# Kernel optimization log

Measured on AMD Instinct MI355X. Metric: run time of the kernel, lower is better.

The kernel has to match this reference:

```python
import jax, jax.numpy as jnp
import numpy as np

N = 100000
IN_DIM = 1280
HID = 128
EPS = 1e-5

def _gconv(x, src, dst, W, b, n):
    # DGL GraphConv, norm='both': D_out^{-1/2} gather -> sum -> D_in^{-1/2}, then W, b.
    # Project first (in_feats >= out_feats here) so edge messages are HID-dim.
    ones = jnp.ones(src.shape[0], dtype=x.dtype)
    out_deg = jnp.clip(jax.ops.segment_sum(ones, src, num_segments=n), 1.0)
    in_deg = jnp.clip(jax.ops.segment_sum(ones, dst, num_segments=n), 1.0)
    h = (x * (out_deg ** -0.5)[:, None]) @ W          # [n, HID]
    agg = jax.ops.segment_sum(h[src], dst, num_segments=n)  # scatter-add over edges
    return agg * (in_deg ** -0.5)[:, None] + b

def _batchnorm(x, g, b):
    m = x.mean(0)
    v = jnp.mean((x - m) ** 2, axis=0)  # biased variance (torch BN normalization)
    return (x - m) * jax.lax.rsqrt(v + EPS) * g + b

def _layer(x, edges, W, b, fcW, fcb, g, beta, n):
    # HeteroGraphConv aggregate='sum' over 3 relations, then FC + ReLU + BN
    h = _gconv(x, edges[0][0], edges[0][1], W[0], b[0], n)
    h = h + _gconv(x, edges[1][0], edges[1][1], W[1], b[1], n)
    h = h + _gconv(x, edges[2][0], edges[2][1], W[2], b[2], n)
    h = h @ fcW + fcb
    h = jax.nn.relu(h)
    return _batchnorm(h, g, beta)

def setup_inputs() -> dict:
    key = jax.random.key(0)
    ks = jax.random.split(key, 16)
    x = jax.random.normal(ks[0], (N, IN_DIM), dtype=jnp.float32)
    seq_edges = jax.random.randint(ks[1], (2, 200000), 0, N, dtype=jnp.int32)
    knn_edges = jax.random.randint(ks[2], (2, 1000000), 0, N, dtype=jnp.int32)
    dis_edges = jax.random.randint(ks[3], (2, 1600000), 0, N, dtype=jnp.int32)
    s_in = 1.0 / np.sqrt(IN_DIM)
    s_h = 1.0 / np.sqrt(HID)
    W0 = jax.random.normal(ks[4], (3, IN_DIM, HID), dtype=jnp.float32) * s_in
    b0 = jnp.zeros((3, HID), dtype=jnp.float32)
    fcW0 = jax.random.normal(ks[5], (HID, HID), dtype=jnp.float32) * s_h
    fcb0 = jnp.zeros((HID,), dtype=jnp.float32)
    g0 = jnp.ones((HID,), dtype=jnp.float32)
    beta0 = jnp.zeros((HID,), dtype=jnp.float32)
    W1 = jax.random.normal(ks[6], (3, HID, HID), dtype=jnp.float32) * s_h
    b1 = jnp.zeros((3, HID), dtype=jnp.float32)
    fcW1 = jax.random.normal(ks[7], (HID, HID), dtype=jnp.float32) * s_h
    fcb1 = jnp.zeros((HID,), dtype=jnp.float32)
    g1 = jnp.ones((HID,), dtype=jnp.float32)
    beta1 = jnp.zeros((HID,), dtype=jnp.float32)
    return {"x": x, "seq_edges": seq_edges, "knn_edges": knn_edges, "dis_edges": dis_edges,
            "W0": W0, "b0": b0, "fcW0": fcW0, "fcb0": fcb0, "g0": g0, "beta0": beta0,
            "W1": W1, "b1": b1, "fcW1": fcW1, "fcb1": fcb1, "g1": g1, "beta1": beta1}

def reference(x, seq_edges, knn_edges, dis_edges,
              W0, b0, fcW0, fcb0, g0, beta0,
              W1, b1, fcW1, fcb1, g1, beta1):
    edges = [seq_edges, knn_edges, dis_edges]
    n = x.shape[0]
    h = _layer(x, edges, W0, b0, fcW0, fcb0, g0, beta0, n)
    # dropout after non-final layers is identity at eval
    h = _layer(h, edges, W1, b1, fcW1, fcb1, g1, beta1, n)
    return h
```

## Files before the change

kernel.cpp:

```cpp
#include <hip/hip_runtime.h>
#include <hip/hip_bf16.h>
#include <math.h>

#define NN 100000
#define HID 128
#define EPSV 1e-5f

typedef short bf16x8 __attribute__((ext_vector_type(8)));
typedef float f32x4 __attribute__((ext_vector_type(4)));
typedef unsigned short u16;

__device__ __forceinline__ u16 f2b(float f) {
  unsigned u = __builtin_bit_cast(unsigned, f);
  u += 0x7FFFu + ((u >> 16) & 1u);
  return (u16)(u >> 16);
}
__device__ __forceinline__ float b2f(u16 h) {
  unsigned u = ((unsigned)h) << 16;
  return __builtin_bit_cast(float, u);
}

#define AS1(p) ((__attribute__((address_space(1))) void*)(p))
#define AS3(p) ((__attribute__((address_space(3))) void*)(p))

static __global__ void k_init(float* __restrict__ degs, int n6,
                              int* __restrict__ cur, int nc,
                              float* __restrict__ stats, int ns) {
  int i = blockIdx.x * blockDim.x + threadIdx.x;
  if (i < n6) degs[i] = 0.f;
  if (i < nc) cur[i] = 0;
  if (i < ns) stats[i] = 0.f;
}

static __global__ void k_deg_all(const int* __restrict__ seq, const int* __restrict__ knn,
                                 const int* __restrict__ dis, int E0, int E1, int E2,
                                 float* __restrict__ sOut, float* __restrict__ sIn) {
  int e = blockIdx.x * blockDim.x + threadIdx.x;
  int rel, eo;
  const int *src, *dst;
  if (e < E0)            { rel = 0; eo = e;           src = seq; dst = seq + E0; }
  else if (e < E0 + E1)  { rel = 1; eo = e - E0;      src = knn; dst = knn + E1; }
  else if (e < E0+E1+E2) { rel = 2; eo = e - E0 - E1; src = dis; dst = dis + E2; }
  else return;
  atomicAdd(&sOut[(size_t)rel * NN + src[eo]], 1.f);
  atomicAdd(&sIn[(size_t)rel * NN + dst[eo]], 1.f);
}

static __global__ void k_scan1_c(const float* __restrict__ indegRaw, int* __restrict__ out,
                                 int* __restrict__ aux, int n) {
  __shared__ int s[256];
  int t = threadIdx.x, i = blockIdx.x * 256 + t;
  int v = 0;
  if (i < NN) v = (int)(indegRaw[i] + indegRaw[NN + i] + indegRaw[2 * NN + i]);
  s[t] = v; __syncthreads();
#pragma unroll
  for (int d = 1; d < 256; d <<= 1) {
    int x = (t >= d) ? s[t - d] : 0;
    __syncthreads();
    s[t] += x;
    __syncthreads();
  }
  if (i < n) out[i] = s[t] - v;
  if (t == 255) aux[blockIdx.x] = s[255];
}

static __global__ void k_scan2(int* __restrict__ aux, int nb) {
  __shared__ int s[256];
  __shared__ int carry;
  int t = threadIdx.x;
  if (t == 0) carry = 0;
  __syncthreads();
  for (int base = 0; base < nb; base += 256) {
    int i = base + t;
    int v = (i < nb) ? aux[i] : 0;
    s[t] = v; __syncthreads();
#pragma unroll
    for (int d = 1; d < 256; d <<= 1) {
      int x = (t >= d) ? s[t - d] : 0;
      __syncthreads();
      s[t] += x;
      __syncthreads();
    }
    int excl = s[t] - v + carry;
    if (i < nb) aux[i] = excl;
    int tot = s[255];
    __syncthreads();
    if (t == 0) carry += tot;
    __syncthreads();
  }
}

static __global__ void k_scan3(int* __restrict__ out, const int* __restrict__ aux, int n) {
  int i = blockIdx.x * 256 + threadIdx.x;
  if (i < n) out[i] += aux[blockIdx.x];
}

static __global__ void k_fill_all(const int* __restrict__ seq, const int* __restrict__ knn,
                                  const int* __restrict__ dis, int E0, int E1, int E2,
                                  const int* __restrict__ off, int* __restrict__ cur,
                                  int* __restrict__ srt) {
  int e = blockIdx.x * blockDim.x + threadIdx.x;
  int rel, eo;
  const int *src, *dst;
  if (e < E0)            { rel = 0; eo = e;           src = seq; dst = seq + E0; }
  else if (e < E0 + E1)  { rel = 1; eo = e - E0;      src = knn; dst = knn + E1; }
  else if (e < E0+E1+E2) { rel = 2; eo = e - E0 - E1; src = dis; dst = dis + E2; }
  else return;
  int d = dst[eo];
  int p = off[d] + atomicAdd(&cur[d], 1);
  srt[p] = (src[eo] << 2) | rel;
}

static __global__ void k_cvt_all(const float* __restrict__ W0, const float* __restrict__ W1,
                                 const float* __restrict__ fcW0, const float* __restrict__ fcW1,
                                 u16* __restrict__ Wt0, u16* __restrict__ Wt1,
                                 u16* __restrict__ fcWt0, u16* __restrict__ fcWt1) {
  const int N0 = 3 * 1280 * 128, N1 = 3 * 128 * 128, N2 = 128 * 128;
  int i = blockIdx.x * blockDim.x + threadIdx.x;
  if (i < N0) {
    int rel = i / (1280 * 128);
    int rem = i - rel * 1280 * 128;
    int k = rem >> 7, c = rem & 127;
    Wt0[((size_t)rel * 128 + c) * 1280 + k] = f2b(W0[i]);
  } else if (i < N0 + N1) {
    int j = i - N0;
    int rel = j / (128 * 128);
    int rem = j - rel * 128 * 128;
    int k = rem >> 7, c = rem & 127;
    Wt1[((size_t)rel * 128 + c) * 128 + k] = f2b(W1[j]);
  } else if (i < N0 + N1 + N2) {
    int j = i - N0 - N1;
    int k = j >> 7, c = j & 127;
    fcWt0[c * 128 + k] = f2b(fcW0[j]);
  } else if (i < N0 + N1 + 2 * N2) {
    int j = i - N0 - N1 - N2;
    int k = j >> 7, c = j & 127;
    fcWt1[c * 128 + k] = f2b(fcW1[j]);
  }
}

template<int K, bool AF32, bool AFFINE>
__global__ __launch_bounds__(512)
void k_gemm_pipe(const void* __restrict__ Av,
                 const u16* __restrict__ Wt,
                 const float* __restrict__ soutRaw,
                 const float* __restrict__ abg,
                 u16* __restrict__ Y,
                 int M)
{
  constexpr int A_BYTES = AF32 ? (128 * 32 * 4) : (128 * 32 * 2);
  constexpr int B_BYTES = 384 * 32 * 2;
  constexpr int BUF_U16 = (A_BYTES + B_BYTES) / 2;
  __shared__ u16 lds[3][BUF_U16];
  __shared__ float abl[256];

  const int row0 = blockIdx.x * 128;
  const int t    = threadIdx.x;
  const int lane = t & 63;
  const int w    = t >> 6;
  const int wm   = w >> 2;
  const int wn   = w & 3;
  const int l15  = lane & 15, l4 = lane >> 4;
  const int kl   = l4 * 8;
  const int nk   = K / 32;

  int ar = row0 + w * 16 + l15;  if (ar >= M) ar = M - 1;

  const float* Af = (const float*)Av;
  const u16*   Ab = (const u16*)Av;

  const u16* gb0 = Wt + (size_t)(w * 48 +      l15) * K + kl;
  const u16* gb1 = Wt + (size_t)(w * 48 + 16 + l15) * K + kl;
  const u16* gb2 = Wt + (size_t)(w * 48 + 32 + l15) * K + kl;

  auto STAGE = [&](int buf, int k0) {
    u16* L = &lds[buf][0];
    if constexpr (AF32) {
      const float* sa = Af + (size_t)ar * K + k0 + kl;
      __builtin_amdgcn_global_load_lds(AS1(sa),     AS3(L + (w * 2048) / 2),          16, 0, 0);
      __builtin_amdgcn_global_load_lds(AS1(sa + 4), AS3(L + (w * 2048 + 1024) / 2),   16, 0, 0);
    } else {
      const u16* sa = Ab + (size_t)ar * K + k0 + kl;
      __builtin_amdgcn_global_load_lds(AS1(sa),     AS3(L + (w * 1024) / 2),          16, 0, 0);
    }
    u16* Bd = L + A_BYTES / 2;
    __builtin_amdgcn_global_load_lds(AS1(gb0 + k0), AS3(Bd + (w * 3 + 0) * 512), 16, 0, 0);
    __builtin_amdgcn_global_load_lds(AS1(gb1 + k0), AS3(Bd + (w * 3 + 1) * 512), 16, 0, 0);
    __builtin_amdgcn_global_load_lds(AS1(gb2 + k0), AS3(Bd + (w * 3 + 2) * 512), 16, 0, 0);
  };

  if constexpr (AFFINE) {
    if (t < 256) abl[t] = abg[t];
  }

  f32x4 acc[4][6];
#pragma unroll
  for (int m = 0; m < 4; ++m)
#pragma unroll
    for (int n = 0; n < 6; ++n) acc[m][n] = (f32x4){0.f, 0.f, 0.f, 0.f};

  STAGE(0, 0);
  if (nk > 1) STAGE(1, 32);

  for (int k = 0; k < nk; ++k) {
    if (k + 1 < nk) {
      if constexpr (AF32) asm volatile("s_waitcnt vmcnt(5)" ::: "memory");
      else                asm volatile("s_waitcnt vmcnt(4)" ::: "memory");
    } else {
      asm volatile("s_waitcnt vmcnt(0)" ::: "memory");
    }
    __builtin_amdgcn_sched_barrier(0);
    __builtin_amdgcn_s_barrier();
    __builtin_amdgcn_sched_barrier(0);

    if (k + 2 < nk) STAGE((k + 2) % 3, (k + 2) * 32);

    const int cur = k % 3;
    const int k0 = k * 32;
    bf16x8 a[4], b[6];
    if constexpr (AF32) {
      f32x4 s1, s2, s3, s4;
      if constexpr (AFFINE) {
        s1 = *(const f32x4*)&abl[k0 + kl];
        s2 = *(const f32x4*)&abl[k0 + kl + 4];
        s3 = *(const f32x4*)&abl[128 + k0 + kl];
        s4 = *(const f32x4*)&abl[128 + k0 + kl + 4];
      }
      const float* Al = (const float*)&lds[cur][0];
#pragma unroll
      for (int m = 0; m < 4; ++m) {
        f32x4 lo = *(const f32x4*)&Al[(wm * 4 + m) * 512 + lane * 4];
        f32x4 hi = *(const f32x4*)&Al[(wm * 4 + m) * 512 + 256 + lane * 4];
        union { bf16x8 v; u16 u[8]; } q;
#pragma unroll
        for (int j = 0; j < 4; ++j) {
          float vlo = lo[j], vhi = hi[j];
          if constexpr (AFFINE) {
            vlo = fmaf(vlo, s1[j], s3[j]);
            vhi = fmaf(vhi, s2[j], s4[j]);
          }
          q.u[j]     = __builtin_bit_cast(u16, __float2bfloat16(vlo));
          q.u[4 + j] = __builtin_bit_cast(u16, __float2bfloat16(vhi));
        }
        a[m] = q.v;
      }
    } else {
      const u16* Al = &lds[cur][0];
#pragma unroll
      for (int m = 0; m < 4; ++m) a[m] = *(const bf16x8*)&Al[(wm * 4 + m) * 512 + lane * 8];
    }
    {
      const u16* Bl = &lds[cur][A_BYTES / 2];
#pragma unroll
      for (int n = 0; n < 6; ++n) b[n] = *(const bf16x8*)&Bl[(wn * 6 + n) * 512 + lane * 8];
    }

#pragma unroll
    for (int m = 0; m < 4; ++m)
#pragma unroll
      for (int n = 0; n < 6; ++n)
        acc[m][n] = __builtin_amdgcn_mfma_f32_16x16x32_bf16(a[m], b[n], acc[m][n], 0, 0, 0);
  }

#pragma unroll
  for (int m = 0; m < 4; ++m) {
    const int rb = row0 + wm * 64 + m * 16 + l4 * 4;
#pragma unroll
    for (int j = 0; j < 4; ++j) {
      const int row = rb + j;
      if (row < M) {
        u16* yrow = Y + (size_t)row * 384;
#pragma unroll
        for (int n = 0; n < 6; ++n) {
          const int c = wn * 96 + n * 16;
          const float sc = rsqrtf(fmaxf(soutRaw[(size_t)(c >> 7) * NN + row], 1.f));
          yrow[c + l15] = f2b(acc[m][n][j] * sc);
        }
      }
    }
  }
}

static __global__ __launch_bounds__(256)
void k_gather(const int* __restrict__ off, const int* __restrict__ srt,
              const float* __restrict__ sinRaw, const u16* __restrict__ Y,
              const float* __restrict__ b, u16* __restrict__ acc16)
{
  int d = blockIdx.x * 4 + (threadIdx.x >> 6);
  if (d >= NN) return;
  int c = (threadIdx.x & 63) * 2;
  float v0 = b[c]     + b[128 + c]     + b[256 + c];
  float v1 = b[c + 1] + b[128 + c + 1] + b[256 + c + 1];
  const float sc0 = rsqrtf(fmaxf(sinRaw[d], 1.f));
  const float sc1 = rsqrtf(fmaxf(sinRaw[NN + d], 1.f));
  const float sc2 = rsqrtf(fmaxf(sinRaw[2 * NN + d], 1.f));
  int j0 = off[d], j1 = off[d + 1];
  int j = j0;
  for (; j + 8 <= j1; j += 8) {
    unsigned uu[8];
    int rr[8];
#pragma unroll
    for (int q = 0; q < 8; ++q) {
      int tg = srt[j + q];
      rr[q] = tg & 3;
      uu[q] = *(const unsigned*)&Y[(size_t)(tg >> 2) * 384 + (size_t)rr[q] * 128 + c];
    }
#pragma unroll
    for (int q = 0; q < 8; ++q) {
      float s = (rr[q] == 0) ? sc0 : ((rr[q] == 1) ? sc1 : sc2);
      v0 = fmaf(b2f((u16)(uu[q] & 0xFFFFu)), s, v0);
      v1 = fmaf(b2f((u16)(uu[q] >> 16)), s, v1);
    }
  }
  for (; j < j1; ++j) {
    int tg = srt[j];
    int r = tg & 3;
    unsigned u = *(const unsigned*)&Y[(size_t)(tg >> 2) * 384 + (size_t)r * 128 + c];
    float s = (r == 0) ? sc0 : ((r == 1) ? sc1 : sc2);
    v0 = fmaf(b2f((u16)(u & 0xFFFFu)), s, v0);
    v1 = fmaf(b2f((u16)(u >> 16)), s, v1);
  }
  unsigned o = (unsigned)f2b(v0) | ((unsigned)f2b(v1) << 16);
  *(unsigned*)&acc16[(size_t)d * 128 + c] = o;
}

static __global__ __launch_bounds__(512)
void k_fc_mfma(const u16* __restrict__ A,
               const u16* __restrict__ Bt,
               const float* __restrict__ bias,
               float* __restrict__ Z, float* __restrict__ stats, int M)
{
  __shared__ u16 Ab[4][4096];
  __shared__ float sst[256];

  const int row0 = blockIdx.x * 128;
  const int t    = threadIdx.x;
  const int lane = t & 63;
  const int w    = t >> 6;
  const int wm   = w >> 2;
  const int wn   = w & 3;
  const int l15  = lane & 15, l4 = lane >> 4;
  const int kl   = l4 * 8;

  if (t < 256) sst[t] = 0.f;

  int ar = row0 + w * 16 + l15;  if (ar >= M) ar = M - 1;

  bf16x8 br[2][4];
#pragma unroll
  for (int n = 0; n < 2; ++n)
#pragma unroll
    for (int ks = 0; ks < 4; ++ks)
      br[n][ks] = *(const bf16x8*)&Bt[(size_t)(wn * 32 + n * 16 + l15) * 128 + ks * 32 + kl];

#pragma unroll
  for (int ks = 0; ks < 4; ++ks)
    __builtin_amdgcn_global_load_lds(AS1(A + (size_t)ar * 128 + ks * 32 + kl),
                                     AS3(&Ab[ks][w * 512]), 16, 0, 0);

  asm volatile("s_waitcnt vmcnt(0)" ::: "memory");
  __syncthreads();

  f32x4 acc[4][2];
#pragma unroll
  for (int m = 0; m < 4; ++m) { acc[m][0] = (f32x4){0,0,0,0}; acc[m][1] = (f32x4){0,0,0,0}; }

#pragma unroll
  for (int ks = 0; ks < 4; ++ks) {
#pragma unroll
    for (int m = 0; m < 4; ++m) {
      bf16x8 a = *(const bf16x8*)&Ab[ks][(wm * 4 + m) * 512 + lane * 8];
      acc[m][0] = __builtin_amdgcn_mfma_f32_16x16x32_bf16(a, br[0][ks], acc[m][0], 0, 0, 0);
      acc[m][1] = __builtin_amdgcn_mfma_f32_16x16x32_bf16(a, br[1][ks], acc[m][1], 0, 0, 0);
    }
  }

  float ps[2] = {0.f, 0.f}, ps2[2] = {0.f, 0.f};
#pragma unroll
  for (int m = 0; m < 4; ++m) {
    const int rb = row0 + wm * 64 + m * 16 + l4 * 4;
#pragma unroll
    for (int j = 0; j < 4; ++j) {
      const int row = rb + j;
      const bool ok = row < M;
#pragma unroll
      for (int n = 0; n < 2; ++n) {
        const int cc = wn * 32 + n * 16 + l15;
        float v = ok ? fmaxf(acc[m][n][j] + bias[cc], 0.f) : 0.f;
        if (ok) Z[(size_t)row * 128 + cc] = v;
        ps[n]  += v;
        ps2[n] += v * v;
      }
    }
  }
#pragma unroll
  for (int n = 0; n < 2; ++n) {
    ps[n]  += __shfl_xor(ps[n], 16);  ps[n]  += __shfl_xor(ps[n], 32);
    ps2[n] += __shfl_xor(ps2[n], 16); ps2[n] += __shfl_xor(ps2[n], 32);
  }
  if (l4 == 0) {
#pragma unroll
    for (int n = 0; n < 2; ++n) {
      const int cc = wn * 32 + n * 16 + l15;
      atomicAdd(&sst[cc], ps[n]);
      atomicAdd(&sst[128 + cc], ps2[n]);
    }
  }
  __syncthreads();
  if (t < 256) atomicAdd(&stats[t], sst[t]);
}

static __global__ void k_bn_finalize(const float* __restrict__ stats, int M,
                                     const float* __restrict__ g, const float* __restrict__ beta,
                                     float* __restrict__ ab) {
  int j = threadIdx.x;
  float m  = stats[j] / (float)M;
  float v  = stats[128 + j] / (float)M - m * m;
  float inv = rsqrtf(v + EPSV) * g[j];
  ab[j]       = inv;
  ab[128 + j] = beta[j] - m * inv;
}

static __global__ void k_bn_apply_f32(const float* __restrict__ Z, const float* __restrict__ ab,
                                      float* __restrict__ out, int n) {
  int i = blockIdx.x * blockDim.x + threadIdx.x;
  if (i < n) {
    int j = i & 127;
    out[i] = Z[i] * ab[j] + ab[128 + j];
  }
}

extern "C" void kernel_launch(void* const* d_in, const int* in_sizes, int n_in,
                              void* d_out, int out_size, void* d_ws, size_t ws_size,
                              hipStream_t stream)
{
  const float* x    = (const float*)d_in[0];
  const int*   seq  = (const int*)d_in[1];
  const int*   knn  = (const int*)d_in[2];
  const int*   dis  = (const int*)d_in[3];
  const float* W0   = (const float*)d_in[4];
  const float* b0   = (const float*)d_in[5];
  const float* fcW0 = (const float*)d_in[6];
  const float* fcb0 = (const float*)d_in[7];
  const float* g0   = (const float*)d_in[8];
  const float* be0  = (const float*)d_in[9];
  const float* W1   = (const float*)d_in[10];
  const float* b1   = (const float*)d_in[11];
  const float* fcW1 = (const float*)d_in[12];
  const float* fcb1 = (const float*)d_in[13];
  const float* g1   = (const float*)d_in[14];
  const float* be1  = (const float*)d_in[15];

  const int E0 = in_sizes[1] / 2, E1 = in_sizes[2] / 2, E2 = in_sizes[3] / 2;
  const int ETOT = E0 + E1 + E2;

  const size_t N = NN;

  float* ws    = (float*)d_ws;
  float* sOut  = ws;
  float* sIn   = sOut + 3 * N;
  u16*   acc16 = (u16*)(sIn + 3 * N);
  float* stats = (float*)(acc16 + N * 128);
  float* ab0   = stats + 512;
  float* ab1   = ab0 + 256;
  u16*   Y     = (u16*)(ab1 + 256);
  float* Z     = (float*)(Y + N * 384);
  u16*   Wt0   = (u16*)(Z + N * 128);
  u16*   Wt1   = Wt0 + 3 * 128 * 1280;
  u16*   fcWt0 = Wt1 + 3 * 128 * 128;
  u16*   fcWt1 = fcWt0 + 128 * 128;
  int*   off   = (int*)(fcWt1 + 128 * 128);
  int*   aux   = off + (NN + 1);
  int*   cur   = aux + 1536;
  int*   srt   = cur + NN;

  const int NT = (NN + 127) / 128;

  k_init<<<(6 * NN + 255) / 256, 256, 0, stream>>>(sOut, 6 * NN, cur, NN, stats, 512);
  k_deg_all<<<(ETOT + 255) / 256, 256, 0, stream>>>(seq, knn, dis, E0, E1, E2, sOut, sIn);

  const int nsc = NN + 1;
  const int nb  = (nsc + 255) / 256;
  k_scan1_c<<<nb, 256, 0, stream>>>(sIn, off, aux, nsc);
  k_scan2<<<1, 256, 0, stream>>>(aux, nb);
  k_scan3<<<nb, 256, 0, stream>>>(off, aux, nsc);

  k_fill_all<<<(ETOT + 255) / 256, 256, 0, stream>>>(seq, knn, dis, E0, E1, E2, off, cur, srt);

  const int CVT_TOT = 3 * 1280 * 128 + 3 * 128 * 128 + 2 * 128 * 128;
  k_cvt_all<<<(CVT_TOT + 255) / 256, 256, 0, stream>>>(W0, W1, fcW0, fcW1, Wt0, Wt1, fcWt0, fcWt1);

  k_gemm_pipe<1280, true, false><<<NT, 512, 0, stream>>>(x, Wt0, sOut, nullptr, Y, NN);
  k_gather<<<(NN + 3) / 4, 256, 0, stream>>>(off, srt, sIn, Y, b0, acc16);
  k_fc_mfma<<<NT, 512, 0, stream>>>(acc16, fcWt0, fcb0, Z, stats, NN);
  k_bn_finalize<<<1, 128, 0, stream>>>(stats, NN, g0, be0, ab0);

  k_gemm_pipe<128, true, true><<<NT, 512, 0, stream>>>(Z, Wt1, sOut, ab0, Y, NN);
  k_gather<<<(NN + 3) / 4, 256, 0, stream>>>(off, srt, sIn, Y, b1, acc16);
  k_fc_mfma<<<NT, 512, 0, stream>>>(acc16, fcWt1, fcb1, Z, stats + 256, NN);
  k_bn_finalize<<<1, 128, 0, stream>>>(stats + 256, NN, g1, be1, ab1);
  k_bn_apply_f32<<<(NN * HID + 255) / 256, 256, 0, stream>>>(Z, ab1, (float*)d_out, NN * HID);
}
```

Measured before the change: 1.090 ms.

## Double GEMM block to 16 waves, halving per-wave N tile

The projection GEMM now runs 1024 threads per block (16 waves in a 2x8 grid) instead of 512, so each wave computes a 64x48 tile with 12 accumulators rather than 64x96. Loading is rebalanced: waves 0-7 stage the A rows plus one B slice, waves 8-15 stage two B slices, and the vmcnt waits are adjusted per wave group. The unused bf16-A path is removed. The aim is more waves to hide latency and fewer registers per wave. The cost is that each A fragment is converted from fp32 in LDS by twice as many waves, and the loads are split unevenly across waves.

```diff
diff --git a/kernel.cpp b/kernel.cpp
--- a/kernel.cpp
+++ b/kernel.cpp
@@ -139,73 +139,66 @@
   }
 }
 
-template<int K, bool AF32, bool AFFINE>
-__global__ __launch_bounds__(512)
-void k_gemm_pipe(const void* __restrict__ Av,
+template<int K, bool AFFINE>
+__global__ __launch_bounds__(1024)
+void k_gemm_pipe(const float* __restrict__ Af,
                  const u16* __restrict__ Wt,
                  const float* __restrict__ soutRaw,
                  const float* __restrict__ abg,
                  u16* __restrict__ Y,
                  int M)
 {
-  constexpr int A_BYTES = AF32 ? (128 * 32 * 4) : (128 * 32 * 2);
-  constexpr int B_BYTES = 384 * 32 * 2;
-  constexpr int BUF_U16 = (A_BYTES + B_BYTES) / 2;
-  __shared__ u16 lds[3][BUF_U16];
+  constexpr int A_U16 = 8192;
+  constexpr int B_U16 = 12288;
+  __shared__ u16 lds[3][A_U16 + B_U16];
   __shared__ float abl[256];
 
   const int row0 = blockIdx.x * 128;
   const int t    = threadIdx.x;
   const int lane = t & 63;
   const int w    = t >> 6;
-  const int wm   = w >> 2;
-  const int wn   = w & 3;
+  const int wm   = w >> 3;
+  const int wn   = w & 7;
   const int l15  = lane & 15, l4 = lane >> 4;
   const int kl   = l4 * 8;
   const int nk   = K / 32;
 
-  int ar = row0 + w * 16 + l15;  if (ar >= M) ar = M - 1;
-
-  const float* Af = (const float*)Av;
-  const u16*   Ab = (const u16*)Av;
-
-  const u16* gb0 = Wt + (size_t)(w * 48 +      l15) * K + kl;
-  const u16* gb1 = Wt + (size_t)(w * 48 + 16 + l15) * K + kl;
-  const u16* gb2 = Wt + (size_t)(w * 48 + 32 + l15) * K + kl;
+  int arA = row0 + w * 16 + l15;  if (arA >= M) arA = M - 1;
+
+  const u16* gbA = Wt + (size_t)(w * 16 + l15) * K + kl;
+  const u16* gbB = Wt + (size_t)((w + 8) * 16 + l15) * K + kl;
 
   auto STAGE = [&](int buf, int k0) {
     u16* L = &lds[buf][0];
-    if constexpr (AF32) {
-      const float* sa = Af + (size_t)ar * K + k0 + kl;
-      __builtin_amdgcn_global_load_lds(AS1(sa),     AS3(L + (w * 2048) / 2),          16, 0, 0);
-      __builtin_amdgcn_global_load_lds(AS1(sa + 4), AS3(L + (w * 2048 + 1024) / 2),   16, 0, 0);
+    if (w < 8) {
+      const float* sa = Af + (size_t)arA * K + k0 + kl;
+      __builtin_amdgcn_global_load_lds(AS1(sa),     AS3(L + w * 1024),       16, 0, 0);
+      __builtin_amdgcn_global_load_lds(AS1(sa + 4), AS3(L + w * 1024 + 512), 16, 0, 0);
+      __builtin_amdgcn_global_load_lds(AS1(gbA + k0), AS3(L + A_U16 + w * 512), 16, 0, 0);
     } else {
-      const u16* sa = Ab + (size_t)ar * K + k0 + kl;
-      __builtin_amdgcn_global_load_lds(AS1(sa),     AS3(L + (w * 1024) / 2),          16, 0, 0);
-    }
-    u16* Bd = L + A_BYTES / 2;
-    __builtin_amdgcn_global_load_lds(AS1(gb0 + k0), AS3(Bd + (w * 3 + 0) * 512), 16, 0, 0);
-    __builtin_amdgcn_global_load_lds(AS1(gb1 + k0), AS3(Bd + (w * 3 + 1) * 512), 16, 0, 0);
-    __builtin_amdgcn_global_load_lds(AS1(gb2 + k0), AS3(Bd + (w * 3 + 2) * 512), 16, 0, 0);
+      __builtin_amdgcn_global_load_lds(AS1(gbA + k0), AS3(L + A_U16 + w * 512),       16, 0, 0);
+      __builtin_amdgcn_global_load_lds(AS1(gbB + k0), AS3(L + A_U16 + (w + 8) * 512), 16, 0, 0);
+    }
   };
 
   if constexpr (AFFINE) {
     if (t < 256) abl[t] = abg[t];
-  }
-
-  f32x4 acc[4][6];
+    asm volatile("s_waitcnt lgkmcnt(0)" ::: "memory");
+  }
+
+  f32x4 acc[4][3];
 #pragma unroll
   for (int m = 0; m < 4; ++m)
 #pragma unroll
-    for (int n = 0; n < 6; ++n) acc[m][n] = (f32x4){0.f, 0.f, 0.f, 0.f};
+    for (int n = 0; n < 3; ++n) acc[m][n] = (f32x4){0.f, 0.f, 0.f, 0.f};
 
   STAGE(0, 0);
   if (nk > 1) STAGE(1, 32);
 
   for (int k = 0; k < nk; ++k) {
     if (k + 1 < nk) {
-      if constexpr (AF32) asm volatile("s_waitcnt vmcnt(5)" ::: "memory");
-      else                asm volatile("s_waitcnt vmcnt(4)" ::: "memory");
+      if (w < 8) asm volatile("s_waitcnt vmcnt(3)" ::: "memory");
+      else       asm volatile("s_waitcnt vmcnt(2)" ::: "memory");
     } else {
       asm volatile("s_waitcnt vmcnt(0)" ::: "memory");
     }
@@ -217,8 +210,8 @@
 
     const int cur = k % 3;
     const int k0 = k * 32;
-    bf16x8 a[4], b[6];
-    if constexpr (AF32) {
+    bf16x8 a[4], b[3];
+    {
       f32x4 s1, s2, s3, s4;
       if constexpr (AFFINE) {
         s1 = *(const f32x4*)&abl[k0 + kl];
@@ -244,21 +237,15 @@
         }
         a[m] = q.v;
       }
-    } else {
-      const u16* Al = &lds[cur][0];
-#pragma unroll
-      for (int m = 0; m < 4; ++m) a[m] = *(const bf16x8*)&Al[(wm * 4 + m) * 512 + lane * 8];
-    }
-    {
-      const u16* Bl = &lds[cur][A_BYTES / 2];
-#pragma unroll
-      for (int n = 0; n < 6; ++n) b[n] = *(const bf16x8*)&Bl[(wn * 6 + n) * 512 + lane * 8];
+      const u16* Bl = &lds[cur][A_U16];
+#pragma unroll
+      for (int n = 0; n < 3; ++n) b[n] = *(const bf16x8*)&Bl[(wn * 3 + n) * 512 + lane * 8];
     }
 
 #pragma unroll
     for (int m = 0; m < 4; ++m)
 #pragma unroll
-      for (int n = 0; n < 6; ++n)
+      for (int n = 0; n < 3; ++n)
         acc[m][n] = __builtin_amdgcn_mfma_f32_16x16x32_bf16(a[m], b[n], acc[m][n], 0, 0, 0);
   }
 
@@ -271,8 +258,8 @@
       if (row < M) {
         u16* yrow = Y + (size_t)row * 384;
 #pragma unroll
-        for (int n = 0; n < 6; ++n) {
-          const int c = wn * 96 + n * 16;
+        for (int n = 0; n < 3; ++n) {
+          const int c = wn * 48 + n * 16;
           const float sc = rsqrtf(fmaxf(soutRaw[(size_t)(c >> 7) * NN + row], 1.f));
           yrow[c + l15] = f2b(acc[m][n][j] * sc);
         }
@@ -490,12 +477,12 @@
   const int CVT_TOT = 3 * 1280 * 128 + 3 * 128 * 128 + 2 * 128 * 128;
   k_cvt_all<<<(CVT_TOT + 255) / 256, 256, 0, stream>>>(W0, W1, fcW0, fcW1, Wt0, Wt1, fcWt0, fcWt1);
 
-  k_gemm_pipe<1280, true, false><<<NT, 512, 0, stream>>>(x, Wt0, sOut, nullptr, Y, NN);
+  k_gemm_pipe<1280, false><<<NT, 1024, 0, stream>>>(x, Wt0, sOut, nullptr, Y, NN);
   k_gather<<<(NN + 3) / 4, 256, 0, stream>>>(off, srt, sIn, Y, b0, acc16);
   k_fc_mfma<<<NT, 512, 0, stream>>>(acc16, fcWt0, fcb0, Z, stats, NN);
   k_bn_finalize<<<1, 128, 0, stream>>>(stats, NN, g0, be0, ab0);
 
-  k_gemm_pipe<128, true, true><<<NT, 512, 0, stream>>>(Z, Wt1, sOut, ab0, Y, NN);
+  k_gemm_pipe<128, true><<<NT, 1024, 0, stream>>>(Z, Wt1, sOut, ab0, Y, NN);
   k_gather<<<(NN + 3) / 4, 256, 0, stream>>>(off, srt, sIn, Y, b1, acc16);
   k_fc_mfma<<<NT, 512, 0, stream>>>(acc16, fcWt1, fcb1, Z, stats + 256, NN);
   k_bn_finalize<<<1, 128, 0, stream>>>(stats + 256, NN, g1, be1, ab1);
```

After: 1.106 ms. Within noise of the previous version (+1.4%).

## Fuse CSR gather aggregation into FC MFMA kernel via swizzled LDS tile

Applied to the files above, without the earlier changes.

Merges the per-node edge gather (scatter-sum over the three relations) with the following FC GEMM. Each 512-thread block aggregates 128 destination rows into a swizzled LDS tile and then runs the MFMA FC from LDS. This removes the bf16 acc16 intermediate round trip through global memory and one launch per layer. In exchange, gather parallelism drops to 781 large blocks each processing 16 rows per wave serially, which may lower latency hiding for the irregular loads. It also drops the unused bf16-A path of the GEMM template and adds an lgkmcnt wait after the affine parameter load.

```diff
diff --git a/kernel.cpp b/kernel.cpp
--- a/kernel.cpp
+++ b/kernel.cpp
@@ -139,16 +139,16 @@
   }
 }
 
-template<int K, bool AF32, bool AFFINE>
+template<int K, bool AFFINE>
 __global__ __launch_bounds__(512)
-void k_gemm_pipe(const void* __restrict__ Av,
+void k_gemm_pipe(const float* __restrict__ Af,
                  const u16* __restrict__ Wt,
                  const float* __restrict__ soutRaw,
                  const float* __restrict__ abg,
                  u16* __restrict__ Y,
                  int M)
 {
-  constexpr int A_BYTES = AF32 ? (128 * 32 * 4) : (128 * 32 * 2);
+  constexpr int A_BYTES = 128 * 32 * 4;
   constexpr int B_BYTES = 384 * 32 * 2;
   constexpr int BUF_U16 = (A_BYTES + B_BYTES) / 2;
   __shared__ u16 lds[3][BUF_U16];
@@ -166,23 +166,15 @@
 
   int ar = row0 + w * 16 + l15;  if (ar >= M) ar = M - 1;
 
-  const float* Af = (const float*)Av;
-  const u16*   Ab = (const u16*)Av;
-
   const u16* gb0 = Wt + (size_t)(w * 48 +      l15) * K + kl;
   const u16* gb1 = Wt + (size_t)(w * 48 + 16 + l15) * K + kl;
   const u16* gb2 = Wt + (size_t)(w * 48 + 32 + l15) * K + kl;
 
   auto STAGE = [&](int buf, int k0) {
     u16* L = &lds[buf][0];
-    if constexpr (AF32) {
-      const float* sa = Af + (size_t)ar * K + k0 + kl;
-      __builtin_amdgcn_global_load_lds(AS1(sa),     AS3(L + (w * 2048) / 2),          16, 0, 0);
-      __builtin_amdgcn_global_load_lds(AS1(sa + 4), AS3(L + (w * 2048 + 1024) / 2),   16, 0, 0);
-    } else {
-      const u16* sa = Ab + (size_t)ar * K + k0 + kl;
-      __builtin_amdgcn_global_load_lds(AS1(sa),     AS3(L + (w * 1024) / 2),          16, 0, 0);
-    }
+    const float* sa = Af + (size_t)ar * K + k0 + kl;
+    __builtin_amdgcn_global_load_lds(AS1(sa),     AS3(L + (w * 2048) / 2),        16, 0, 0);
+    __builtin_amdgcn_global_load_lds(AS1(sa + 4), AS3(L + (w * 2048 + 1024) / 2), 16, 0, 0);
     u16* Bd = L + A_BYTES / 2;
     __builtin_amdgcn_global_load_lds(AS1(gb0 + k0), AS3(Bd + (w * 3 + 0) * 512), 16, 0, 0);
     __builtin_amdgcn_global_load_lds(AS1(gb1 + k0), AS3(Bd + (w * 3 + 1) * 512), 16, 0, 0);
@@ -191,6 +183,7 @@
 
   if constexpr (AFFINE) {
     if (t < 256) abl[t] = abg[t];
+    asm volatile("s_waitcnt lgkmcnt(0)" ::: "memory");
   }
 
   f32x4 acc[4][6];
@@ -203,12 +196,8 @@
   if (nk > 1) STAGE(1, 32);
 
   for (int k = 0; k < nk; ++k) {
-    if (k + 1 < nk) {
-      if constexpr (AF32) asm volatile("s_waitcnt vmcnt(5)" ::: "memory");
-      else                asm volatile("s_waitcnt vmcnt(4)" ::: "memory");
-    } else {
-      asm volatile("s_waitcnt vmcnt(0)" ::: "memory");
-    }
+    if (k + 1 < nk) asm volatile("s_waitcnt vmcnt(5)" ::: "memory");
+    else            asm volatile("s_waitcnt vmcnt(0)" ::: "memory");
     __builtin_amdgcn_sched_barrier(0);
     __builtin_amdgcn_s_barrier();
     __builtin_amdgcn_sched_barrier(0);
@@ -218,7 +207,7 @@
     const int cur = k % 3;
     const int k0 = k * 32;
     bf16x8 a[4], b[6];
-    if constexpr (AF32) {
+    {
       f32x4 s1, s2, s3, s4;
       if constexpr (AFFINE) {
         s1 = *(const f32x4*)&abl[k0 + kl];
@@ -244,12 +233,6 @@
         }
         a[m] = q.v;
       }
-    } else {
-      const u16* Al = &lds[cur][0];
-#pragma unroll
-      for (int m = 0; m < 4; ++m) a[m] = *(const bf16x8*)&Al[(wm * 4 + m) * 512 + lane * 8];
-    }
-    {
       const u16* Bl = &lds[cur][A_BYTES / 2];
 #pragma unroll
       for (int n = 0; n < 6; ++n) b[n] = *(const bf16x8*)&Bl[(wn * 6 + n) * 512 + lane * 8];
@@ -281,70 +264,73 @@
   }
 }
 
-static __global__ __launch_bounds__(256)
-void k_gather(const int* __restrict__ off, const int* __restrict__ srt,
-              const float* __restrict__ sinRaw, const u16* __restrict__ Y,
-              const float* __restrict__ b, u16* __restrict__ acc16)
+static __global__ __launch_bounds__(512)
+void k_gfc(const int* __restrict__ off, const int* __restrict__ srt,
+           const float* __restrict__ sinRaw, const u16* __restrict__ Y,
+           const float* __restrict__ b,
+           const u16* __restrict__ Bt, const float* __restrict__ bias,
+           float* __restrict__ Z, float* __restrict__ stats, int M)
 {
-  int d = blockIdx.x * 4 + (threadIdx.x >> 6);
-  if (d >= NN) return;
-  int c = (threadIdx.x & 63) * 2;
-  float v0 = b[c]     + b[128 + c]     + b[256 + c];
-  float v1 = b[c + 1] + b[128 + c + 1] + b[256 + c + 1];
-  const float sc0 = rsqrtf(fmaxf(sinRaw[d], 1.f));
-  const float sc1 = rsqrtf(fmaxf(sinRaw[NN + d], 1.f));
-  const float sc2 = rsqrtf(fmaxf(sinRaw[2 * NN + d], 1.f));
-  int j0 = off[d], j1 = off[d + 1];
-  int j = j0;
-  for (; j + 8 <= j1; j += 8) {
-    unsigned uu[8];
-    int rr[8];
-#pragma unroll
-    for (int q = 0; q < 8; ++q) {
-      int tg = srt[j + q];
-      rr[q] = tg & 3;
-      uu[q] = *(const unsigned*)&Y[(size_t)(tg >> 2) * 384 + (size_t)rr[q] * 128 + c];
-    }
-#pragma unroll
-    for (int q = 0; q < 8; ++q) {
-      float s = (rr[q] == 0) ? sc0 : ((rr[q] == 1) ? sc1 : sc2);
-      v0 = fmaf(b2f((u16)(uu[q] & 0xFFFFu)), s, v0);
-      v1 = fmaf(b2f((u16)(uu[q] >> 16)), s, v1);
-    }
-  }
-  for (; j < j1; ++j) {
-    int tg = srt[j];
-    int r = tg & 3;
-    unsigned u = *(const unsigned*)&Y[(size_t)(tg >> 2) * 384 + (size_t)r * 128 + c];
-    float s = (r == 0) ? sc0 : ((r == 1) ? sc1 : sc2);
-    v0 = fmaf(b2f((u16)(u & 0xFFFFu)), s, v0);
-    v1 = fmaf(b2f((u16)(u >> 16)), s, v1);
-  }
-  unsigned o = (unsigned)f2b(v0) | ((unsigned)f2b(v1) << 16);
-  *(unsigned*)&acc16[(size_t)d * 128 + c] = o;
-}
-
-static __global__ __launch_bounds__(512)
-void k_fc_mfma(const u16* __restrict__ A,
-               const u16* __restrict__ Bt,
-               const float* __restrict__ bias,
-               float* __restrict__ Z, float* __restrict__ stats, int M)
-{
-  __shared__ u16 Ab[4][4096];
+  __shared__ unsigned Ablk[128 * 64];
   __shared__ float sst[256];
 
-  const int row0 = blockIdx.x * 128;
   const int t    = threadIdx.x;
   const int lane = t & 63;
   const int w    = t >> 6;
-  const int wm   = w >> 2;
-  const int wn   = w & 3;
-  const int l15  = lane & 15, l4 = lane >> 4;
-  const int kl   = l4 * 8;
+  const int row0 = blockIdx.x * 128;
 
   if (t < 256) sst[t] = 0.f;
 
-  int ar = row0 + w * 16 + l15;  if (ar >= M) ar = M - 1;
+  {
+    const int c = lane * 2;
+    const float bb0 = b[c]     + b[128 + c]     + b[256 + c];
+    const float bb1 = b[c + 1] + b[128 + c + 1] + b[256 + c + 1];
+    for (int i = 0; i < 16; ++i) {
+      const int r = w * 16 + i;
+      const int d = row0 + r;
+      float v0 = 0.f, v1 = 0.f;
+      if (d < M) {
+        v0 = bb0; v1 = bb1;
+        const float sc0 = rsqrtf(fmaxf(sinRaw[d], 1.f));
+        const float sc1 = rsqrtf(fmaxf(sinRaw[NN + d], 1.f));
+        const float sc2 = rsqrtf(fmaxf(sinRaw[2 * NN + d], 1.f));
+        int j0 = off[d], j1 = off[d + 1];
+        int j = j0;
+        for (; j + 8 <= j1; j += 8) {
+          unsigned uu[8];
+          int rr[8];
+#pragma unroll
+          for (int q = 0; q < 8; ++q) {
+            int tg = srt[j + q];
+            rr[q] = tg & 3;
+            uu[q] = *(const unsigned*)&Y[(size_t)(tg >> 2) * 384 + (size_t)rr[q] * 128 + c];
+          }
+#pragma unroll
+          for (int q = 0; q < 8; ++q) {
+            float s = (rr[q] == 0) ? sc0 : ((rr[q] == 1) ? sc1 : sc2);
+            v0 = fmaf(b2f((u16)(uu[q] & 0xFFFFu)), s, v0);
+            v1 = fmaf(b2f((u16)(uu[q] >> 16)), s, v1);
+          }
+        }
+        for (; j < j1; ++j) {
+          int tg = srt[j];
+          int rl = tg & 3;
+          unsigned u = *(const unsigned*)&Y[(size_t)(tg >> 2) * 384 + (size_t)rl * 128 + c];
+          float s = (rl == 0) ? sc0 : ((rl == 1) ? sc1 : sc2);
+          v0 = fmaf(b2f((u16)(u & 0xFFFFu)), s, v0);
+          v1 = fmaf(b2f((u16)(u >> 16)), s, v1);
+        }
+      }
+      unsigned o = (unsigned)f2b(v0) | ((unsigned)f2b(v1) << 16);
+      unsigned ba = (unsigned)(r * 256 + lane * 4) ^ ((unsigned)(r & 7) << 4);
+      Ablk[ba >> 2] = o;
+    }
+  }
+  __syncthreads();
+
+  const int wm = w >> 2, wn = w & 3;
+  const int l15 = lane & 15, l4 = lane >> 4;
+  const int kl = l4 * 8;
 
   bf16x8 br[2][4];
 #pragma unroll
@@ -353,14 +339,6 @@
     for (int ks = 0; ks < 4; ++ks)
       br[n][ks] = *(const bf16x8*)&Bt[(size_t)(wn * 32 + n * 16 + l15) * 128 + ks * 32 + kl];
 
-#pragma unroll
-  for (int ks = 0; ks < 4; ++ks)
-    __builtin_amdgcn_global_load_lds(AS1(A + (size_t)ar * 128 + ks * 32 + kl),
-                                     AS3(&Ab[ks][w * 512]), 16, 0, 0);
-
-  asm volatile("s_waitcnt vmcnt(0)" ::: "memory");
-  __syncthreads();
-
   f32x4 acc[4][2];
 #pragma unroll
   for (int m = 0; m < 4; ++m) { acc[m][0] = (f32x4){0,0,0,0}; acc[m][1] = (f32x4){0,0,0,0}; }
@@ -369,7 +347,9 @@
   for (int ks = 0; ks < 4; ++ks) {
 #pragma unroll
     for (int m = 0; m < 4; ++m) {
-      bf16x8 a = *(const bf16x8*)&Ab[ks][(wm * 4 + m) * 512 + lane * 8];
+      const int r = (wm * 4 + m) * 16 + l15;
+      unsigned ba = (unsigned)(r * 256 + ks * 64 + l4 * 16) ^ ((unsigned)(r & 7) << 4);
+      bf16x8 a = *(const bf16x8*)((const char*)Ablk + ba);
       acc[m][0] = __builtin_amdgcn_mfma_f32_16x16x32_bf16(a, br[0][ks], acc[m][0], 0, 0, 0);
       acc[m][1] = __builtin_amdgcn_mfma_f32_16x16x32_bf16(a, br[1][ks], acc[m][1], 0, 0, 0);
     }
@@ -459,8 +439,7 @@
   float* ws    = (float*)d_ws;
   float* sOut  = ws;
   float* sIn   = sOut + 3 * N;
-  u16*   acc16 = (u16*)(sIn + 3 * N);
-  float* stats = (float*)(acc16 + N * 128);
+  float* stats = sIn + 3 * N;
   float* ab0   = stats + 512;
   float* ab1   = ab0 + 256;
   u16*   Y     = (u16*)(ab1 + 256);
@@ -490,14 +469,12 @@
   const int CVT_TOT = 3 * 1280 * 128 + 3 * 128 * 128 + 2 * 128 * 128;
   k_cvt_all<<<(CVT_TOT + 255) / 256, 256, 0, stream>>>(W0, W1, fcW0, fcW1, Wt0, Wt1, fcWt0, fcWt1);
 
-  k_gemm_pipe<1280, true, false><<<NT, 512, 0, stream>>>(x, Wt0, sOut, nullptr, Y, NN);
-  k_gather<<<(NN + 3) / 4, 256, 0, stream>>>(off, srt, sIn, Y, b0, acc16);
-  k_fc_mfma<<<NT, 512, 0, stream>>>(acc16, fcWt0, fcb0, Z, stats, NN);
+  k_gemm_pipe<1280, false><<<NT, 512, 0, stream>>>(x, Wt0, sOut, nullptr, Y, NN);
+  k_gfc<<<NT, 512, 0, stream>>>(off, srt, sIn, Y, b0, fcWt0, fcb0, Z, stats, NN);
   k_bn_finalize<<<1, 128, 0, stream>>>(stats, NN, g0, be0, ab0);
 
-  k_gemm_pipe<128, true, true><<<NT, 512, 0, stream>>>(Z, Wt1, sOut, ab0, Y, NN);
-  k_gather<<<(NN + 3) / 4, 256, 0, stream>>>(off, srt, sIn, Y, b1, acc16);
-  k_fc_mfma<<<NT, 512, 0, stream>>>(acc16, fcWt1, fcb1, Z, stats + 256, NN);
+  k_gemm_pipe<128, true><<<NT, 512, 0, stream>>>(Z, Wt1, sOut, ab0, Y, NN);
+  k_gfc<<<NT, 512, 0, stream>>>(off, srt, sIn, Y, b1, fcWt1, fcb1, Z, stats + 256, NN);
   k_bn_finalize<<<1, 128, 0, stream>>>(stats + 256, NN, g1, be1, ab1);
   k_bn_apply_f32<<<(NN * HID + 255) / 256, 256, 0, stream>>>(Z, ab1, (float*)d_out, NN * HID);
 }
```

Result: slower. 1.232 ms (+13.0%).
